# Kernel tuning notes

Measured on AMD Instinct MI355X. Metric: run time of the kernel, lower is better.

Reference implementation:

```python
import jax, jax.numpy as jnp
import numpy as np

B, F0, D = 4096, 39, 16
CIN = [128, 128, 128]


def setup_inputs() -> dict:
    key = jax.random.key(0)
    ks = jax.random.split(key, 4)
    x = jax.random.normal(ks[0], (B, F0, D), dtype=jnp.float32)
    fields = [F0] + CIN
    inp = {"embedded_features": x}
    for i in range(len(CIN)):
        cin = F0 * fields[i]
        cout = fields[i + 1]
        kw = jax.random.fold_in(ks[1], i)
        # Conv1d default init scale ~ 1/sqrt(fan_in)
        inp[f"W{i}"] = jax.random.normal(kw, (cout, cin), dtype=jnp.float32) / np.sqrt(cin)
        inp[f"b{i}"] = jnp.zeros((cout,), dtype=jnp.float32)
    return inp


def _cin_layer(X0, Xi, W, b):
    # Math identical to: outer_product [B,F0,Fi,D] -> reshape [B,F0*Fi,D] -> 1x1 Conv1d.
    # Conv1d(kernel=1) over the flattened F0*Fi channel dim is a contraction over (j,k):
    #   Xn[b,h,d] = sum_{j,k} W[h, j*Fi+k] * X0[b,j,d] * Xi[b,k,d] + b[h]
    H = W.shape[0]
    F0_, Fi = X0.shape[1], Xi.shape[1]
    Wr = W.reshape(H, F0_, Fi)
    return jnp.einsum('hjk,bjd,bkd->bhd', Wr, X0, Xi) + b[None, :, None]


def reference(embedded_features, W0, b0, W1, b1, W2, b2):
    X0 = embedded_features  # [B, F0, D]
    Ws = [(W0, b0), (W1, b1), (W2, b2)]
    Xi = X0
    res = []
    for W, b in Ws:
        Xi = _cin_layer(X0, Xi, W, b)  # [B, H_i, D]
        res.append(Xi.sum(axis=2))     # sum over embedding dim
    return jnp.concatenate(res, axis=1)  # [B, sum(cin_size)]
```

## Files before the change

### kernel.cpp

```cpp
#include <hip/hip_runtime.h>
#include <stdint.h>


#define NB_F0 39
#define NB_H  128
#define NB_B  4096

typedef float f32x4  __attribute__((ext_vector_type(4)));
typedef float f32x16 __attribute__((ext_vector_type(16)));
typedef short s16x8  __attribute__((ext_vector_type(8)));

__device__ __forceinline__ void dma16(const void* g, void* l) {
  __builtin_amdgcn_global_load_lds(
      (const __attribute__((address_space(1))) unsigned int*)g,
      (__attribute__((address_space(3))) unsigned int*)l, 16, 0, 0);
}

__device__ __forceinline__ unsigned short rne_bf16(float f) {
  union { float f; unsigned u; } v; v.f = f;
  return (unsigned short)((v.u + 0x7fffu + ((v.u >> 16) & 1u)) >> 16);
}
__device__ __forceinline__ float bf16_to_f32(unsigned short s) {
  union { unsigned u; float f; } v; v.u = ((unsigned)s) << 16;
  return v.f;
}

__global__ void prep_x0_kernel(const float* __restrict__ X0g,
                               unsigned short* __restrict__ X0T,
                               unsigned short* __restrict__ X0c) {
  const int b = blockIdx.x;
  const int t = threadIdx.x;
  {
    const int d  = t >> 4;
    const int k4 = (t & 15) << 2;
    unsigned short vv[4];
#pragma unroll
    for (int i = 0; i < 4; ++i) {
      const int k = k4 + i;
      vv[i] = (k < NB_F0) ? rne_bf16(X0g[(size_t)b * (NB_F0 * 16) + k * 16 + d])
                          : (unsigned short)0;
    }
    ushort4 pk; pk.x = vv[0]; pk.y = vv[1]; pk.z = vv[2]; pk.w = vv[3];
    *(ushort4*)&X0T[((size_t)b * 16 + d) * 64 + k4] = pk;
  }
  for (int idx = t; idx < NB_F0 * 16; idx += 256) {
    const int j = idx >> 4, pos = idx & 15;
    const int d = (pos & 3) | (((pos >> 3) & 1) << 2) | (((pos >> 2) & 1) << 3);
    X0c[(size_t)b * (NB_F0 * 16) + idx] =
        rne_bf16(X0g[(size_t)b * (NB_F0 * 16) + j * 16 + d]);
  }
}

__global__ void prep_w_kernel(const float* __restrict__ Wsrc,
                              unsigned short* __restrict__ Wdst,
                              int Fi, int kshift, int total) {
  int idx = blockIdx.x * 256 + threadIdx.x;
  if (idx >= total) return;
  const int i    = idx & 7;
  const int lane = (idx >> 3) & 63;
  const int c    = (idx >> 9) & ((1 << kshift) - 1);
  const int jt   = idx >> (9 + kshift);
  const int t    = jt & 3;
  const int j    = jt >> 2;
  const int h = t * 32 + (lane & 31);
  const int k = c * 16 + ((lane >> 5) << 3) + i;
  unsigned short v = 0;
  if (k < Fi) v = rne_bf16(Wsrc[(size_t)h * (NB_F0 * Fi) + j * Fi + k]);
  Wdst[idx] = v;
}

template <int FI_PAD, bool STORE_XN>
__global__ __launch_bounds__(256, 2) void cin_layer(
    const unsigned short* __restrict__ Wf,
    const unsigned short* __restrict__ XiT,
    const unsigned short* __restrict__ X0c,
    const float* __restrict__ bias,
    unsigned short* __restrict__ XnT,
    float* __restrict__ outp)
{
  constexpr int KPASS = FI_PAD / 64;
  constexpr int KC16  = FI_PAD / 16;
  constexpr int S     = NB_F0 * KPASS;

  __shared__ __attribute__((aligned(16))) unsigned short Wlds[2][2048];
  __shared__ __attribute__((aligned(16))) unsigned short x0s[32 * NB_F0 * 16];

  const int tid  = threadIdx.x;
  const int lane = tid & 63;
  const int wv   = tid >> 6;
  const int L    = lane >> 5;
  const int col  = lane & 31;
  const int ht   = blockIdx.x >> 7;
  const int bblk = (blockIdx.x & 127) * 32;
  const int bwave = bblk + wv * 8;

  auto dma_stage = [&](int s, int buf) {
    const int pass = (KPASS == 2 && s >= NB_F0) ? 1 : 0;
    const int j = s - pass * NB_F0;
    const unsigned short* src =
        Wf + (((size_t)(j * 4 + ht) * KC16) + pass * 4 + wv) * 512 + lane * 8;
    dma16(src, &Wlds[buf][wv * 512]);
  };

  {
    const unsigned short* src = X0c + (size_t)bblk * (NB_F0 * 16);
    for (int c = tid; c < (32 * NB_F0 * 16) / 8; c += 256)
      *(s16x8*)&x0s[c * 8] = *(const s16x8*)&src[c * 8];
  }
  dma_stage(0, 0);

  s16x8 af[4][4];
  auto load_af = [&](int pass) {
#pragma unroll
    for (int P = 0; P < 4; ++P) {
      const unsigned short* base = XiT +
          ((size_t)(bwave + 2 * P + (col >> 4)) * 16 + (col & 15)) * FI_PAD +
          pass * 64 + L * 8;
#pragma unroll
      for (int c = 0; c < 4; ++c) af[P][c] = *(const s16x8*)(base + c * 16);
    }
  };
  load_af(0);

  f32x16 Xacc[4], kZero;
#pragma unroll
  for (int r = 0; r < 16; ++r) kZero[r] = 0.f;
#pragma unroll
  for (int P = 0; P < 4; ++P) Xacc[P] = kZero;

  const int x0base = (wv * 8) * (NB_F0 * 16) + L * 8;

  for (int s = 0; s < S; ++s) {
    __syncthreads();
    if (s + 1 < S) dma_stage(s + 1, (s + 1) & 1);
    if (KPASS == 2 && s == NB_F0) load_af(1);

    const int j = (KPASS == 2 && s >= NB_F0) ? s - NB_F0 : s;
    const unsigned short* wb = &Wlds[s & 1][lane * 8];
    const s16x8 w0 = *(const s16x8*)(wb);
    const s16x8 w1 = *(const s16x8*)(wb + 512);
    const s16x8 w2 = *(const s16x8*)(wb + 1024);
    const s16x8 w3 = *(const s16x8*)(wb + 1536);

#pragma unroll
    for (int P = 0; P < 4; ++P) {
      f32x16 y;
      y = __builtin_amdgcn_mfma_f32_32x32x16_bf16(af[P][0], w0, kZero, 0, 0, 0);
      y = __builtin_amdgcn_mfma_f32_32x32x16_bf16(af[P][1], w1, y, 0, 0, 0);
      y = __builtin_amdgcn_mfma_f32_32x32x16_bf16(af[P][2], w2, y, 0, 0, 0);
      y = __builtin_amdgcn_mfma_f32_32x32x16_bf16(af[P][3], w3, y, 0, 0, 0);

      const uint4 xu0 = *(const uint4*)
          &x0s[x0base + (2 * P + 0) * (NB_F0 * 16) + j * 16];
      const uint4 xu1 = *(const uint4*)
          &x0s[x0base + (2 * P + 1) * (NB_F0 * 16) + j * 16];
      const unsigned wd[8] = {xu0.x, xu0.y, xu0.z, xu0.w,
                              xu1.x, xu1.y, xu1.z, xu1.w};
      f32x16 xsc;
#pragma unroll
      for (int i = 0; i < 8; ++i) {
        xsc[2 * i]     = __uint_as_float(wd[i] << 16);
        xsc[2 * i + 1] = __uint_as_float(wd[i] & 0xffff0000u);
      }
      Xacc[P] = __builtin_elementwise_fma(xsc, y, Xacc[P]);
    }
  }

  const float bias_v = bias[ht * 32 + col];
#pragma unroll
  for (int P = 0; P < 4; ++P) {
#pragma unroll
    for (int bh = 0; bh < 2; ++bh) {
      const int b = bwave + 2 * P + bh;
      float v[8];
#pragma unroll
      for (int m = 0; m < 8; ++m) v[m] = Xacc[P][bh * 8 + m] + bias_v;
      if (STORE_XN) {
#pragma unroll
        for (int m = 0; m < 8; ++m) {
          const int d = (m & 3) + 8 * ((m >> 2) & 1) + 4 * L;
          XnT[((size_t)b * 16 + d) * NB_H + ht * 32 + col] = rne_bf16(v[m]);
        }
      }
      float tot = ((v[0] + v[1]) + (v[2] + v[3])) + ((v[4] + v[5]) + (v[6] + v[7]));
      tot += __shfl_xor(tot, 32);
      if (lane < 32) outp[(size_t)b * 384 + ht * 32 + lane] = tot;
    }
  }
}

extern "C" void kernel_launch(void* const* d_in, const int* in_sizes, int n_in,
                              void* d_out, int out_size, void* d_ws, size_t ws_size,
                              hipStream_t stream) {
  (void)in_sizes; (void)n_in; (void)out_size; (void)ws_size;
  const float* X0g = (const float*)d_in[0];
  const float* W0  = (const float*)d_in[1];
  const float* b0  = (const float*)d_in[2];
  const float* W1  = (const float*)d_in[3];
  const float* b1  = (const float*)d_in[4];
  const float* W2  = (const float*)d_in[5];
  const float* b2  = (const float*)d_in[6];
  float* out = (float*)d_out;

  char* p = (char*)d_ws;
  unsigned short* X0T = (unsigned short*)p; p += (size_t)NB_B * 16 * 64 * 2;
  unsigned short* X0c = (unsigned short*)p; p += (size_t)NB_B * NB_F0 * 16 * 2;
  unsigned short* X1T = (unsigned short*)p; p += (size_t)NB_B * 16 * 128 * 2;
  unsigned short* X2T = (unsigned short*)p; p += (size_t)NB_B * 16 * 128 * 2;
  unsigned short* Wf0 = (unsigned short*)p; p += (size_t)NB_F0 * 4 * 4 * 512 * 2;
  unsigned short* Wf1 = (unsigned short*)p; p += (size_t)NB_F0 * 4 * 8 * 512 * 2;
  unsigned short* Wf2 = (unsigned short*)p; p += (size_t)NB_F0 * 4 * 8 * 512 * 2;

  hipLaunchKernelGGL(prep_x0_kernel, dim3(NB_B), dim3(256), 0, stream,
                     X0g, X0T, X0c);
  const int tw0  = NB_F0 * 4 * 4 * 512;
  const int tw12 = NB_F0 * 4 * 8 * 512;
  hipLaunchKernelGGL(prep_w_kernel, dim3((tw0 + 255) / 256), dim3(256), 0, stream,
                     W0, Wf0, 39, 2, tw0);
  hipLaunchKernelGGL(prep_w_kernel, dim3((tw12 + 255) / 256), dim3(256), 0, stream,
                     W1, Wf1, 128, 3, tw12);
  hipLaunchKernelGGL(prep_w_kernel, dim3((tw12 + 255) / 256), dim3(256), 0, stream,
                     W2, Wf2, 128, 3, tw12);

  hipLaunchKernelGGL((cin_layer<64, true>),   dim3(512), dim3(256), 0, stream,
                     Wf0, X0T, X0c, b0, X1T, out + 0);
  hipLaunchKernelGGL((cin_layer<128, true>),  dim3(512), dim3(256), 0, stream,
                     Wf1, X1T, X0c, b1, X2T, out + 128);
  hipLaunchKernelGGL((cin_layer<128, false>), dim3(512), dim3(256), 0, stream,
                     Wf2, X2T, X0c, b2, (unsigned short*)nullptr, out + 256);
}
```

Measured before the change: 316.3 us.

## Read X0 scale factors from global fp32 and deepen weight DMA pipeline

Removes the per-block LDS staging of X0 (about 40KB of shared memory). Each lane now reads pre-widened fp32 X0 values straight from global memory inside the MFMA loop. The weight LDS ring grows from 2 to 4 buffers, and the loop handles two stages per barrier, halving the number of __syncthreads. Freeing LDS should allow more blocks per CU, at the cost of doubling X0 global traffic and putting global-load latency inside the inner loop.

```diff
diff --git a/kernel.cpp b/kernel.cpp
--- a/kernel.cpp
+++ b/kernel.cpp
@@ -27,7 +27,7 @@
 
 __global__ void prep_x0_kernel(const float* __restrict__ X0g,
                                unsigned short* __restrict__ X0T,
-                               unsigned short* __restrict__ X0c) {
+                               float* __restrict__ X0f) {
   const int b = blockIdx.x;
   const int t = threadIdx.x;
   {
@@ -46,8 +46,8 @@
   for (int idx = t; idx < NB_F0 * 16; idx += 256) {
     const int j = idx >> 4, pos = idx & 15;
     const int d = (pos & 3) | (((pos >> 3) & 1) << 2) | (((pos >> 2) & 1) << 3);
-    X0c[(size_t)b * (NB_F0 * 16) + idx] =
-        rne_bf16(X0g[(size_t)b * (NB_F0 * 16) + j * 16 + d]);
+    X0f[(size_t)b * (NB_F0 * 16) + idx] =
+        bf16_to_f32(rne_bf16(X0g[(size_t)b * (NB_F0 * 16) + j * 16 + d]));
   }
 }
 
@@ -73,7 +73,7 @@
 __global__ __launch_bounds__(256, 2) void cin_layer(
     const unsigned short* __restrict__ Wf,
     const unsigned short* __restrict__ XiT,
-    const unsigned short* __restrict__ X0c,
+    const float* __restrict__ X0f,
     const float* __restrict__ bias,
     unsigned short* __restrict__ XnT,
     float* __restrict__ outp)
@@ -82,8 +82,7 @@
   constexpr int KC16  = FI_PAD / 16;
   constexpr int S     = NB_F0 * KPASS;
 
-  __shared__ __attribute__((aligned(16))) unsigned short Wlds[2][2048];
-  __shared__ __attribute__((aligned(16))) unsigned short x0s[32 * NB_F0 * 16];
+  __shared__ __attribute__((aligned(16))) unsigned short Wlds[4][2048];
 
   const int tid  = threadIdx.x;
   const int lane = tid & 63;
@@ -102,13 +101,6 @@
     dma16(src, &Wlds[buf][wv * 512]);
   };
 
-  {
-    const unsigned short* src = X0c + (size_t)bblk * (NB_F0 * 16);
-    for (int c = tid; c < (32 * NB_F0 * 16) / 8; c += 256)
-      *(s16x8*)&x0s[c * 8] = *(const s16x8*)&src[c * 8];
-  }
-  dma_stage(0, 0);
-
   s16x8 af[4][4];
   auto load_af = [&](int pass) {
 #pragma unroll
@@ -128,15 +120,11 @@
 #pragma unroll
   for (int P = 0; P < 4; ++P) Xacc[P] = kZero;
 
-  const int x0base = (wv * 8) * (NB_F0 * 16) + L * 8;
-
-  for (int s = 0; s < S; ++s) {
-    __syncthreads();
-    if (s + 1 < S) dma_stage(s + 1, (s + 1) & 1);
-    if (KPASS == 2 && s == NB_F0) load_af(1);
-
+  const float* const x0w = X0f + (size_t)bwave * (NB_F0 * 16) + L * 8;
+
+  auto stage = [&](int s) {
     const int j = (KPASS == 2 && s >= NB_F0) ? s - NB_F0 : s;
-    const unsigned short* wb = &Wlds[s & 1][lane * 8];
+    const unsigned short* wb = &Wlds[s & 3][lane * 8];
     const s16x8 w0 = *(const s16x8*)(wb);
     const s16x8 w1 = *(const s16x8*)(wb + 512);
     const s16x8 w2 = *(const s16x8*)(wb + 1024);
@@ -150,20 +138,32 @@
       y = __builtin_amdgcn_mfma_f32_32x32x16_bf16(af[P][2], w2, y, 0, 0, 0);
       y = __builtin_amdgcn_mfma_f32_32x32x16_bf16(af[P][3], w3, y, 0, 0, 0);
 
-      const uint4 xu0 = *(const uint4*)
-          &x0s[x0base + (2 * P + 0) * (NB_F0 * 16) + j * 16];
-      const uint4 xu1 = *(const uint4*)
-          &x0s[x0base + (2 * P + 1) * (NB_F0 * 16) + j * 16];
-      const unsigned wd[8] = {xu0.x, xu0.y, xu0.z, xu0.w,
-                              xu1.x, xu1.y, xu1.z, xu1.w};
+      const float* xp = x0w + ((size_t)(2 * P) * NB_F0 + j) * 16;
+      const f32x4 a0 = *(const f32x4*)(xp);
+      const f32x4 a1 = *(const f32x4*)(xp + 4);
+      const f32x4 b0 = *(const f32x4*)(xp + NB_F0 * 16);
+      const f32x4 b1 = *(const f32x4*)(xp + NB_F0 * 16 + 4);
       f32x16 xsc;
 #pragma unroll
-      for (int i = 0; i < 8; ++i) {
-        xsc[2 * i]     = __uint_as_float(wd[i] << 16);
-        xsc[2 * i + 1] = __uint_as_float(wd[i] & 0xffff0000u);
+      for (int i = 0; i < 4; ++i) {
+        xsc[i] = a0[i]; xsc[4 + i] = a1[i];
+        xsc[8 + i] = b0[i]; xsc[12 + i] = b1[i];
       }
       Xacc[P] = __builtin_elementwise_fma(xsc, y, Xacc[P]);
     }
+  };
+
+  dma_stage(0, 0);
+  if (S > 1) dma_stage(1, 1);
+  constexpr int NSTEP = (S + 1) / 2;
+  for (int t = 0; t < NSTEP; ++t) {
+    __syncthreads();
+    const int s0 = 2 * t;
+    if (s0 + 2 < S) dma_stage(s0 + 2, (s0 + 2) & 3);
+    if (s0 + 3 < S) dma_stage(s0 + 3, (s0 + 3) & 3);
+    stage(s0);
+    if (KPASS == 2 && s0 + 1 == NB_F0) load_af(1);
+    if (s0 + 1 < S) stage(s0 + 1);
   }
 
   const float bias_v = bias[ht * 32 + col];
@@ -204,7 +204,7 @@
 
   char* p = (char*)d_ws;
   unsigned short* X0T = (unsigned short*)p; p += (size_t)NB_B * 16 * 64 * 2;
-  unsigned short* X0c = (unsigned short*)p; p += (size_t)NB_B * NB_F0 * 16 * 2;
+  float*          X0f = (float*)p;          p += (size_t)NB_B * NB_F0 * 16 * 4;
   unsigned short* X1T = (unsigned short*)p; p += (size_t)NB_B * 16 * 128 * 2;
   unsigned short* X2T = (unsigned short*)p; p += (size_t)NB_B * 16 * 128 * 2;
   unsigned short* Wf0 = (unsigned short*)p; p += (size_t)NB_F0 * 4 * 4 * 512 * 2;
@@ -212,7 +212,7 @@
   unsigned short* Wf2 = (unsigned short*)p; p += (size_t)NB_F0 * 4 * 8 * 512 * 2;
 
   hipLaunchKernelGGL(prep_x0_kernel, dim3(NB_B), dim3(256), 0, stream,
-                     X0g, X0T, X0c);
+                     X0g, X0T, X0f);
   const int tw0  = NB_F0 * 4 * 4 * 512;
   const int tw12 = NB_F0 * 4 * 8 * 512;
   hipLaunchKernelGGL(prep_w_kernel, dim3((tw0 + 255) / 256), dim3(256), 0, stream,
@@ -223,9 +223,9 @@
                      W2, Wf2, 128, 3, tw12);
 
   hipLaunchKernelGGL((cin_layer<64, true>),   dim3(512), dim3(256), 0, stream,
-                     Wf0, X0T, X0c, b0, X1T, out + 0);
+                     Wf0, X0T, X0f, b0, X1T, out + 0);
   hipLaunchKernelGGL((cin_layer<128, true>),  dim3(512), dim3(256), 0, stream,
-                     Wf1, X1T, X0c, b1, X2T, out + 128);
+                     Wf1, X1T, X0f, b1, X2T, out + 128);
   hipLaunchKernelGGL((cin_layer<128, false>), dim3(512), dim3(256), 0, stream,
-                     Wf2, X2T, X0c, b2, (unsigned short*)nullptr, out + 256);
-}
+                     Wf2, X2T, X0f, b2, (unsigned short*)nullptr, out + 256);
+}
```

Measured after the change: 493.5 us. +56.0%, slower.
